# Optimization experiments

Hardware: AMD Instinct MI355X
Metric: run time of the kernel (lower is better)

Reference implementation:

```python
import jax, jax.numpy as jnp
import numpy as np

HIDDEN = 2048
N_HEADS = 16
HEAD_DIM = HIDDEN // N_HEADS
SEQ = 4096
ROPE_BASE = 10000.0


def setup_inputs() -> dict:
    key = jax.random.key(0)
    ks = jax.random.split(key, 5)
    sc = 1.0 / np.sqrt(HIDDEN)
    return {
        "hidden_states": jax.random.normal(ks[0], (SEQ, HIDDEN), jnp.float32),
        "Wq": jax.random.normal(ks[1], (HIDDEN, HIDDEN), jnp.float32) * sc,
        "Wk": jax.random.normal(ks[2], (HIDDEN, HIDDEN), jnp.float32) * sc,
        "Wv": jax.random.normal(ks[3], (HIDDEN, HIDDEN), jnp.float32) * sc,
        "Wo": jax.random.normal(ks[4], (HIDDEN, HIDDEN), jnp.float32) * sc,
    }


def _rope_cos_sin(seq_len, head_dim, dtype):
    # Llama-style rotary embedding tables, shape [S, 1, head_dim]
    inv_freq = 1.0 / (ROPE_BASE ** (jnp.arange(0, head_dim, 2, dtype=jnp.float32) / head_dim))
    pos = jnp.arange(seq_len, dtype=jnp.float32)
    freqs = pos[:, None] * inv_freq[None, :]          # [S, d/2]
    emb = jnp.concatenate([freqs, freqs], axis=-1)     # [S, d]
    return jnp.cos(emb)[:, None, :].astype(dtype), jnp.sin(emb)[:, None, :].astype(dtype)


def _rotate_half(x):
    h = x.shape[-1] // 2
    return jnp.concatenate([-x[..., h:], x[..., :h]], axis=-1)


def reference(hidden_states, Wq, Wk, Wv, Wo):
    S, H = hidden_states.shape
    d = HEAD_DIM
    # QKV projections (nn.Linear: x @ W.T), split into heads: [S, nH, d]
    q = (hidden_states @ Wq.T).reshape(S, N_HEADS, d)
    k = (hidden_states @ Wk.T).reshape(S, N_HEADS, d)
    v = (hidden_states @ Wv.T).reshape(S, N_HEADS, d)
    # Per-position RoPE on q and k
    cos, sin = _rope_cos_sin(S, d, q.dtype)
    q = q * cos + _rotate_half(q) * sin
    k = k * cos + _rotate_half(k) * sin
    # Causal scaled-dot-product attention, scores [nH, S, S]
    scores = jnp.einsum("snd,tnd->nst", q, k) / jnp.sqrt(jnp.asarray(d, q.dtype))
    causal = jnp.tril(jnp.ones((S, S), dtype=bool))
    scores = jnp.where(causal[None, :, :], scores, jnp.asarray(-1e30, scores.dtype))
    probs = jax.nn.softmax(scores, axis=-1)
    ctx = jnp.einsum("nst,tnd->snd", probs, v).reshape(S, H)
    return ctx @ Wo.T
```

## Files before the change

### kernel.cpp

```cpp
#include <hip/hip_runtime.h>

#define SEQ 4096
#define HIDDEN 2048
#define NHEADS 16
#define HDIM 128
#define QBLK 128
#define KVB 64

typedef float f32x4 __attribute__((ext_vector_type(4)));
typedef __bf16 bf16x8 __attribute__((ext_vector_type(8)));
typedef unsigned int u32x4 __attribute__((ext_vector_type(4)));
typedef unsigned short u16x8 __attribute__((ext_vector_type(8)));
typedef unsigned short u16;

#define SCL2 0.12751747456918851f
#define RLOG 0.2076205059304601f

__device__ __forceinline__ u16 f2bf(float f) {
  unsigned u = __float_as_uint(f);
  unsigned r = 0x7fffu + ((u >> 16) & 1u);
  return (u16)((u + r) >> 16);
}
__device__ __forceinline__ float bf2f(u16 u) {
  return __uint_as_float(((unsigned)u) << 16);
}
__device__ __forceinline__ unsigned cvtpk(float a, float b) {
  unsigned r;
  asm volatile("v_cvt_pk_bf16_f32 %0, %1, %2" : "=v"(r) : "v"(a), "v"(b));
  return r;
}

__device__ __forceinline__ void gload16(const u16* g, u16* l) {
  __builtin_amdgcn_global_load_lds(
      (const __attribute__((address_space(1))) unsigned int*)g,
      (__attribute__((address_space(3))) unsigned int*)l, 16, 0, 0);
}

__device__ __forceinline__ int cumq(int q) {
  return q < 24 ? (q - 12) * 2 : 24 + (q - 24) * 3;
}

__global__ __launch_bounds__(256) void cvt5(const float* __restrict__ X,
    const float* __restrict__ Wq, const float* __restrict__ Wk,
    const float* __restrict__ Wv, const float* __restrict__ Wo,
    u16* __restrict__ dst) {
  const size_t SH = (size_t)SEQ * HIDDEN, HH = (size_t)HIDDEN * HIDDEN;
  size_t i = ((size_t)blockIdx.x * 256 + threadIdx.x) * 8;
  const float* src; size_t off;
  if (i < SH) { src = X; off = i; }
  else if (i < SH + HH) { src = Wq; off = i - SH; }
  else if (i < SH + 2 * HH) { src = Wk; off = i - SH - HH; }
  else if (i < SH + 3 * HH) { src = Wv; off = i - SH - 2 * HH; }
  else { src = Wo; off = i - SH - 3 * HH; }
  float4 a = *reinterpret_cast<const float4*>(src + off);
  float4 b = *reinterpret_cast<const float4*>(src + off + 4);
  u16x8 o;
  o[0] = f2bf(a.x); o[1] = f2bf(a.y); o[2] = f2bf(a.z); o[3] = f2bf(a.w);
  o[4] = f2bf(b.x); o[5] = f2bf(b.y); o[6] = f2bf(b.z); o[7] = f2bf(b.w);
  *reinterpret_cast<u32x4*>(dst + i) = __builtin_bit_cast(u32x4, o);
}

__global__ __launch_bounds__(256, 3) void gemm_qkv(const u16* __restrict__ Xb,
    const u16* __restrict__ Wqb, const u16* __restrict__ Wkb,
    const u16* __restrict__ Wvb, u16* __restrict__ Qo, u16* __restrict__ Ko,
    u16* __restrict__ Vt) {
  __shared__ u16 As[3][4096];
  __shared__ u16 Bs[3][4096];
  const int wg = blockIdx.x;
  const int swz = (wg & 7) * 192 + (wg >> 3);
  const int z = swz >> 9;
  const int rr_ = swz & 511;
  const u16 *A, *B;
  u16* C;
  int bm, bn, cst;
  if (z == 2) {
    A = Wvb; B = Xb; C = Vt;
    bm = (rr_ & 15) << 7; bn = (rr_ >> 4) << 7; cst = SEQ;
  } else {
    A = Xb; B = z ? Wkb : Wqb; C = z ? Ko : Qo;
    bm = (rr_ & 31) << 7; bn = (rr_ >> 5) << 7; cst = HIDDEN;
  }
  const int t = threadIdx.x, lane = t & 63, wave = t >> 6;
  const int lrow = lane & 15, lgrp = lane >> 4;
  const int wr = (wave >> 1) * 64;
  const int wc = (wave & 1) * 64;
  const int r0 = t >> 2;
  const int c0 = ((t & 3) ^ ((r0 >> 1) & 3)) * 8;
  const int ksx8 = (lgrp ^ ((lrow >> 1) & 3)) * 8;

  f32x4 acc[4][4] = {};

  const u16* Ab = A + (size_t)(bm + r0) * HIDDEN + c0;
  const int nr0 = (z < 2)
      ? (((r0 >> 4) >> 1) * 16 + (r0 & 15) + ((r0 >> 4) & 1) * 64)
      : r0;
  const u16* Bb = B + (size_t)(bn + nr0) * HIDDEN + c0;
  const size_t rstepA = (size_t)64 * HIDDEN;
  const size_t rstepB = (size_t)((z < 2) ? 32 : 64) * HIDDEN;

#define QKV_STAGE(tt, s)                                            \
  {                                                                 \
    const int ko = (tt) * 32;                                       \
    gload16(Ab + ko, &As[s][t * 8]);                                \
    gload16(Bb + ko, &Bs[s][t * 8]);                                \
    gload16(Ab + rstepA + ko, &As[s][2048 + t * 8]);                \
    gload16(Bb + rstepB + ko, &Bs[s][2048 + t * 8]);                \
  }

  QKV_STAGE(0, 0);
  QKV_STAGE(1, 1);
  asm volatile("s_waitcnt vmcnt(4)" ::: "memory");
  __builtin_amdgcn_s_barrier();
  asm volatile("" ::: "memory");

  int sa = 0, sb = 1, sc = 2;
  for (int tt = 0; tt < 64; ++tt) {
    if (tt + 2 < 64) QKV_STAGE(tt + 2, sc);
    bf16x8 af[4], bfv[4];
#pragma unroll
    for (int mf = 0; mf < 4; ++mf)
      af[mf] = __builtin_bit_cast(bf16x8,
          *reinterpret_cast<const u32x4*>(&As[sa][(wr + mf * 16 + lrow) * 32 + ksx8]));
#pragma unroll
    for (int nf = 0; nf < 4; ++nf)
      bfv[nf] = __builtin_bit_cast(bf16x8,
          *reinterpret_cast<const u32x4*>(&Bs[sa][(wc + nf * 16 + lrow) * 32 + ksx8]));
#pragma unroll
    for (int nf = 0; nf < 4; ++nf)
#pragma unroll
      for (int mf = 0; mf < 4; ++mf)
        acc[mf][nf] = __builtin_amdgcn_mfma_f32_16x16x32_bf16(af[mf], bfv[nf], acc[mf][nf], 0, 0, 0);
    asm volatile("s_waitcnt vmcnt(4)" ::: "memory");
    __builtin_amdgcn_sched_barrier(0);
    __builtin_amdgcn_s_barrier();
    asm volatile("" ::: "memory");
    int s_ = sa; sa = sb; sb = sc; sc = s_;
  }
#undef QKV_STAGE

  const int rb = lgrp * 4;
  if (z < 2) {
    const float qscale = (z == 0) ? SCL2 : 1.0f;
#pragma unroll
    for (int mf = 0; mf < 4; ++mf)
#pragma unroll
      for (int j = 0; j < 2; ++j) {
        const int ii = (((wc >> 4) + 2 * j) >> 1) * 16 + lrow;
        const float inv = exp2f((float)ii * -RLOG);
#pragma unroll
        for (int qq = 0; qq < 4; ++qq) {
          const int s = bm + wr + mf * 16 + rb + qq;
          float ang = (float)s * inv;
          float sn, cs;
          __sincosf(ang, &sn, &cs);
          sn *= qscale; cs *= qscale;
          float x1 = acc[mf][2 * j][qq], x2 = acc[mf][2 * j + 1][qq];
          C[(size_t)s * cst + bn + ii] = f2bf(x1 * cs - x2 * sn);
          C[(size_t)s * cst + bn + ii + 64] = f2bf(x2 * cs + x1 * sn);
        }
      }
  } else {
#pragma unroll
    for (int mf = 0; mf < 4; ++mf)
#pragma unroll
      for (int nf = 0; nf < 4; ++nf) {
        const int col = bn + wc + ((nf >> 1) & 1) * 32 + (lrow >> 2) * 8 +
                        (nf & 1) * 4 + (lrow & 3);
#pragma unroll
        for (int qq = 0; qq < 4; ++qq) {
          const int s = bm + wr + mf * 16 + rb + qq;
          C[(size_t)s * cst + col] = f2bf(acc[mf][nf][qq]);
        }
      }
  }
}

__global__ __launch_bounds__(256, 3) void gemm_out(const u16* __restrict__ A,
    const u16* __restrict__ B, float* __restrict__ C) {
  __shared__ u16 As[3][4096];
  __shared__ u16 Bs[3][4096];
  const int wg = blockIdx.x;
  const int swz = (wg & 7) * 64 + (wg >> 3);
  const int bm = (swz & 31) << 7;
  const int bn = (swz >> 5) << 7;
  const int t = threadIdx.x, lane = t & 63, wave = t >> 6;
  const int lrow = lane & 15, lgrp = lane >> 4;
  const int wr = (wave >> 1) * 64;
  const int wc = (wave & 1) * 64;
  const int r0 = t >> 2;
  const int c0 = ((t & 3) ^ ((r0 >> 1) & 3)) * 8;
  const int ksx8 = (lgrp ^ ((lrow >> 1) & 3)) * 8;

  f32x4 acc[4][4] = {};

  const u16* Ab = A + (size_t)(bm + r0) * HIDDEN + c0;
  const u16* Bb = B + (size_t)(bn + r0) * HIDDEN + c0;
  const size_t rstep = (size_t)64 * HIDDEN;

#define OUT_STAGE(tt, s)                                            \
  {                                                                 \
    const int ko = (tt) * 32;                                       \
    gload16(Ab + ko, &As[s][t * 8]);                                \
    gload16(Bb + ko, &Bs[s][t * 8]);                                \
    gload16(Ab + rstep + ko, &As[s][2048 + t * 8]);                 \
    gload16(Bb + rstep + ko, &Bs[s][2048 + t * 8]);                 \
  }

  OUT_STAGE(0, 0);
  OUT_STAGE(1, 1);
  asm volatile("s_waitcnt vmcnt(4)" ::: "memory");
  __builtin_amdgcn_s_barrier();
  asm volatile("" ::: "memory");

  int sa = 0, sb = 1, sc = 2;
  for (int tt = 0; tt < 64; ++tt) {
    if (tt + 2 < 64) OUT_STAGE(tt + 2, sc);
    bf16x8 af[4], bfv[4];
#pragma unroll
    for (int mf = 0; mf < 4; ++mf)
      af[mf] = __builtin_bit_cast(bf16x8,
          *reinterpret_cast<const u32x4*>(&As[sa][(wr + mf * 16 + lrow) * 32 + ksx8]));
#pragma unroll
    for (int nf = 0; nf < 4; ++nf)
      bfv[nf] = __builtin_bit_cast(bf16x8,
          *reinterpret_cast<const u32x4*>(&Bs[sa][(wc + nf * 16 + lrow) * 32 + ksx8]));
#pragma unroll
    for (int nf = 0; nf < 4; ++nf)
#pragma unroll
      for (int mf = 0; mf < 4; ++mf)
        acc[mf][nf] = __builtin_amdgcn_mfma_f32_16x16x32_bf16(af[mf], bfv[nf], acc[mf][nf], 0, 0, 0);
    asm volatile("s_waitcnt vmcnt(4)" ::: "memory");
    __builtin_amdgcn_sched_barrier(0);
    __builtin_amdgcn_s_barrier();
    asm volatile("" ::: "memory");
    int s_ = sa; sa = sb; sb = sc; sc = s_;
  }
#undef OUT_STAGE

  const int rb = lgrp * 4;
#pragma unroll
  for (int mf = 0; mf < 4; ++mf)
#pragma unroll
    for (int nf = 0; nf < 4; ++nf)
#pragma unroll
      for (int qq = 0; qq < 4; ++qq)
        C[(size_t)(bm + wr + mf * 16 + rb + qq) * HIDDEN + bn + wc + nf * 16 + lrow] =
            acc[mf][nf][qq];
}

__global__ __launch_bounds__(512, 4) void attn_kernel(const u16* __restrict__ Q,
                                                      const u16* __restrict__ Kg,
                                                      const u16* __restrict__ Vt,
                                                      u16* __restrict__ O,
                                                      u16* __restrict__ Opart,
                                                      float* __restrict__ Ml) {
  __shared__ u16 Ks[2][KVB * 128];
  __shared__ u16 Vs[2][128 * KVB];
  const int t = threadIdx.x;
  const int wave = t >> 6;
  const int lane = t & 63;
  const int lrow = lane & 15;
  const int lgrp = lane >> 4;

  const int g = blockIdx.x;
  const int h = g & 15;
  const int e = g >> 4;
  int q, c, nc;
  if (e < 24)      { q = 24 + e / 3;           c = e % 3;         nc = 3; }
  else if (e < 48) { q = 23 - ((e - 24) >> 1); c = (e - 24) & 1;  nc = 2; }
  else             { q = 59 - e;               c = 0;             nc = 1; }
  const int total = 2 * q + 2;
  const int base = total / nc, rem = total - base * nc;
  const int it0 = c * base + (c < rem ? c : rem);
  const int it1 = it0 + base + (c < rem ? 1 : 0);

  const int qw = q * QBLK + wave * 16;

  bf16x8 qf[4];
#pragma unroll
  for (int kk = 0; kk < 4; ++kk)
    qf[kk] = __builtin_bit_cast(bf16x8, *reinterpret_cast<const u32x4*>(
        Q + (size_t)(qw + lrow) * HIDDEN + h * HDIM + kk * 32 + lgrp * 8));

  u16x8 ow;
#pragma unroll
  for (int j = 0; j < 8; ++j) ow[j] = (lrow == 0) ? 0x3F80 : 0;
  const bf16x8 vones = __builtin_bit_cast(bf16x8, ow);

  const u16* kgb[2]; const u16* vgb[2]; int kof[2], vof[2];
#pragma unroll
  for (int is = 0; is < 2; ++is) {
    int ch = is * 512 + t;
    int krow = ch >> 4, kslot = ch & 15;
    int kcol = ((kslot & 8) | ((kslot ^ krow) & 7)) * 8;
    kgb[is] = Kg + (size_t)krow * HIDDEN + h * HDIM + kcol;
    kof[is] = ch * 8;
    int vrow = ch >> 3, vslot = ch & 7;
    int vcol = ((vslot ^ vrow) & 7) * 8;
    vgb[is] = Vt + (size_t)(h * HDIM + vrow) * SEQ + vcol;
    vof[is] = ch * 8;
  }

  f32x4 acc[8] = {};
  f32x4 acc1 = {};
  float m2 = -1e30f;

#pragma unroll
  for (int is = 0; is < 2; ++is) {
    gload16(kgb[is] + (size_t)(it0 * KVB) * HIDDEN, &Ks[0][kof[is]]);
    gload16(vgb[is] + it0 * KVB, &Vs[0][vof[is]]);
  }
  __syncthreads();

  int p = 0;
  for (int bt = it0; bt < it1; ++bt) {
    const int t0 = bt * KVB;
    if (bt + 1 < it1) {
      const int t1 = (bt + 1) * KVB;
#pragma unroll
      for (int is = 0; is < 2; ++is) {
        gload16(kgb[is] + (size_t)t1 * HIDDEN, &Ks[p ^ 1][kof[is]]);
        gload16(vgb[is] + t1, &Vs[p ^ 1][vof[is]]);
      }
    }

    if (t0 <= qw + 15) {
      const bool need_mask = (t0 + KVB - 1 > qw);
      f32x4 sc[4] = {};
      __builtin_amdgcn_s_setprio(1);
#pragma unroll
      for (int kk = 0; kk < 4; ++kk) {
#pragma unroll
        for (int colf = 0; colf < 4; ++colf) {
          int trow = colf * 16 + lrow;
          int slot = kk * 4 + lgrp;
          bf16x8 kf = __builtin_bit_cast(bf16x8, *reinterpret_cast<const u32x4*>(
              &Ks[p][trow * 128 + ((slot & 8) | ((slot ^ trow) & 7)) * 8]));
          sc[colf] = __builtin_amdgcn_mfma_f32_16x16x32_bf16(kf, qf[kk], sc[colf], 0, 0, 0);
        }
      }
      __builtin_amdgcn_s_setprio(0);

      const int qg = qw + lrow;
      if (need_mask) {
#pragma unroll
        for (int colf = 0; colf < 4; ++colf) {
          const int kvb0 = t0 + colf * 16 + lgrp * 4;
#pragma unroll
          for (int r = 0; r < 4; ++r)
            sc[colf][r] = (kvb0 + r <= qg) ? sc[colf][r] : -1e30f;
        }
      }
      float mc[4];
#pragma unroll
      for (int colf = 0; colf < 4; ++colf)
        mc[colf] = fmaxf(fmaxf(sc[colf][0], sc[colf][1]),
                         fmaxf(sc[colf][2], sc[colf][3]));
      float mx = fmaxf(fmaxf(mc[0], mc[1]), fmaxf(mc[2], mc[3]));
      mx = fmaxf(mx, __shfl_xor(mx, 16));
      mx = fmaxf(mx, __shfl_xor(mx, 32));

      if (__any(mx > m2 + 11.5f)) {
        float mn = fmaxf(m2, mx);
        float sf = exp2f(m2 - mn);
        m2 = mn;
#pragma unroll
        for (int r = 0; r < 4; ++r) {
          float sfr = __shfl(sf, (lane & 48) | (lgrp * 4 + r));
#pragma unroll
          for (int nn = 0; nn < 8; ++nn) acc[nn][r] *= sfr;
          acc1[r] *= sfr;
        }
      }

      unsigned paw[2][4];
#pragma unroll
      for (int colf = 0; colf < 4; ++colf) {
        float pv[4];
#pragma unroll
        for (int r = 0; r < 4; ++r) pv[r] = exp2f(sc[colf][r] - m2);
        paw[colf >> 1][(colf & 1) * 2 + 0] = cvtpk(pv[0], pv[1]);
        paw[colf >> 1][(colf & 1) * 2 + 1] = cvtpk(pv[2], pv[3]);
      }

      __builtin_amdgcn_s_setprio(1);
#pragma unroll
      for (int ks = 0; ks < 2; ++ks) {
        u32x4 w = {paw[ks][0], paw[ks][1], paw[ks][2], paw[ks][3]};
        bf16x8 pa = __builtin_bit_cast(bf16x8, w);
#pragma unroll
        for (int nn = 0; nn < 8; ++nn) {
          const int d = nn * 16 + lrow;
          bf16x8 vb = __builtin_bit_cast(bf16x8, *reinterpret_cast<const u32x4*>(
              &Vs[p][d * 64 + (((ks * 4 + lgrp) ^ d) & 7) * 8]));
          acc[nn] = __builtin_amdgcn_mfma_f32_16x16x32_bf16(pa, vb, acc[nn], 0, 0, 0);
        }
        acc1 = __builtin_amdgcn_mfma_f32_16x16x32_bf16(pa, vones, acc1, 0, 0, 0);
      }
      __builtin_amdgcn_s_setprio(0);
    }

    __syncthreads();
    p ^= 1;
  }

  if (nc == 1) {
    float inv[4];
#pragma unroll
    for (int r = 0; r < 4; ++r)
      inv[r] = 1.0f / __shfl(acc1[r], lane & 48);
#pragma unroll
    for (int nn = 0; nn < 8; ++nn)
#pragma unroll
      for (int r = 0; r < 4; ++r) {
        int row = qw + lgrp * 4 + r;
        int col = h * HDIM + nn * 16 + lrow;
        O[(size_t)row * HIDDEN + col] = f2bf(acc[nn][r] * inv[r]);
      }
  } else {
    const int slot = h * 48 + cumq(q) + c;
    u16* Op = Opart + (size_t)slot * (QBLK * HDIM);
    float* ml = Ml + (size_t)slot * 256;
#pragma unroll
    for (int nn = 0; nn < 8; ++nn)
#pragma unroll
      for (int r = 0; r < 4; ++r) {
        int rl = wave * 16 + lgrp * 4 + r;
        Op[rl * HDIM + nn * 16 + lrow] = f2bf(acc[nn][r]);
      }
    if (lgrp == 0) {
      int rl = wave * 16 + lrow;
      ml[rl] = m2;
    }
    if (lrow == 0) {
#pragma unroll
      for (int r = 0; r < 4; ++r)
        ml[128 + wave * 16 + lgrp * 4 + r] = acc1[r];
    }
  }
}

__global__ __launch_bounds__(256) void combine_kernel(const u16* __restrict__ Opart,
                                                      const float* __restrict__ Ml,
                                                      u16* __restrict__ O) {
  const int bid = blockIdx.x;
  const int h = bid / 20;
  const int q = 12 + bid % 20;
  const int nc = (q < 24) ? 2 : 3;
  const int sbase = h * 48 + cumq(q);
  const int r = threadIdx.x >> 1;
  const int d0 = (threadIdx.x & 1) * 64;

  float w[3], l = 0.f, M = -3.0e38f;
#pragma unroll
  for (int c = 0; c < 3; ++c)
    if (c < nc) M = fmaxf(M, Ml[(size_t)(sbase + c) * 256 + r]);
#pragma unroll
  for (int c = 0; c < 3; ++c)
    if (c < nc) {
      w[c] = exp2f(Ml[(size_t)(sbase + c) * 256 + r] - M);
      l += w[c] * Ml[(size_t)(sbase + c) * 256 + 128 + r];
    }
  const float inv = 1.0f / l;

  for (int dd = 0; dd < 64; dd += 8) {
    float a8[8] = {};
#pragma unroll
    for (int c = 0; c < 3; ++c)
      if (c < nc) {
        u16x8 v = *reinterpret_cast<const u16x8*>(
            Opart + (size_t)(sbase + c) * (QBLK * HDIM) + r * HDIM + d0 + dd);
#pragma unroll
        for (int j = 0; j < 8; ++j) a8[j] += w[c] * bf2f(v[j]);
      }
    u16x8 o8;
#pragma unroll
    for (int j = 0; j < 8; ++j) o8[j] = f2bf(a8[j] * inv);
    *reinterpret_cast<u16x8*>(
        &O[(size_t)(q * QBLK + r) * HIDDEN + h * HDIM + d0 + dd]) = o8;
  }
}

extern "C" void kernel_launch(void* const* d_in, const int* in_sizes, int n_in,
                              void* d_out, int out_size, void* d_ws, size_t ws_size,
                              hipStream_t stream) {
  const float* X  = (const float*)d_in[0];
  const float* Wq = (const float*)d_in[1];
  const float* Wk = (const float*)d_in[2];
  const float* Wv = (const float*)d_in[3];
  const float* Wo = (const float*)d_in[4];
  float* out = (float*)d_out;

  u16* ws = (u16*)d_ws;
  const size_t SH = (size_t)SEQ * HIDDEN;
  const size_t HH = (size_t)HIDDEN * HIDDEN;
  u16* Xb  = ws;
  u16* Wqb = Xb + SH;
  u16* Wkb = Wqb + HH;
  u16* Wvb = Wkb + HH;
  u16* Wob = Wvb + HH;
  u16* Qb  = Wob + HH;
  u16* Kb  = Qb + SH;
  u16* Vtb = Kb + SH;
  u16* Cb  = Vtb + SH;

  u16* Opart = ws;
  float* Ml = (float*)(ws + (size_t)768 * 16384);

  cvt5<<<(int)((SH + 4 * HH) / 2048), 256, 0, stream>>>(X, Wq, Wk, Wv, Wo, ws);

  gemm_qkv<<<1536, 256, 0, stream>>>(Xb, Wqb, Wkb, Wvb, Qb, Kb, Vtb);

  attn_kernel<<<960, 512, 0, stream>>>(Qb, Kb, Vtb, Cb, Opart, Ml);
  combine_kernel<<<320, 256, 0, stream>>>(Opart, Ml, Cb);

  gemm_out<<<512, 256, 0, stream>>>(Cb, Wob, out);
}
```

Before: 323.1 us.

## Double attention query tile to 256 rows with two row fragments per wave

Each wave of the attention kernel now handles 32 query rows (two 16-row fragments) instead of 16, so every K/V tile loaded into shared memory feeds twice as many MFMAs. The split-KV schedule is rebuilt for 16 query tiles per head with up to 4 chunks, and the combine kernel and workspace layout are resized to match. This halves K/V traffic per query but doubles accumulator registers per wave, which may reduce occupancy under the 512x4 launch bounds, and it leaves fewer blocks (640 instead of 960).

Result: slower. 514.8 us (+59.3%).

```diff
diff --git a/kernel.cpp b/kernel.cpp
--- a/kernel.cpp
+++ b/kernel.cpp
@@ -4,7 +4,6 @@
 #define HIDDEN 2048
 #define NHEADS 16
 #define HDIM 128
-#define QBLK 128
 #define KVB 64
 
 typedef float f32x4 __attribute__((ext_vector_type(4)));
@@ -37,7 +36,9 @@
 }
 
 __device__ __forceinline__ int cumq(int q) {
-  return q < 24 ? (q - 12) * 2 : 24 + (q - 24) * 3;
+  if (q < 8) return (q - 4) * 2;
+  if (q < 12) return 8 + (q - 8) * 3;
+  return 20 + (q - 12) * 4;
 }
 
 __global__ __launch_bounds__(256) void cvt5(const float* __restrict__ X,
@@ -265,51 +266,46 @@
   const int g = blockIdx.x;
   const int h = g & 15;
   const int e = g >> 4;
-  int q, c, nc;
-  if (e < 24)      { q = 24 + e / 3;           c = e % 3;         nc = 3; }
-  else if (e < 48) { q = 23 - ((e - 24) >> 1); c = (e - 24) & 1;  nc = 2; }
-  else             { q = 59 - e;               c = 0;             nc = 1; }
-  const int total = 2 * q + 2;
+  int qt, c, nc;
+  if (e < 16)      { qt = 15 - (e >> 2);        c = e & 3;         nc = 4; }
+  else if (e < 28) { qt = 11 - (e - 16) / 3;    c = (e - 16) % 3;  nc = 3; }
+  else if (e < 36) { qt = 7 - ((e - 28) >> 1);  c = (e - 28) & 1;  nc = 2; }
+  else             { qt = 39 - e;               c = 0;             nc = 1; }
+  const int total = 4 * (qt + 1);
   const int base = total / nc, rem = total - base * nc;
   const int it0 = c * base + (c < rem ? c : rem);
   const int it1 = it0 + base + (c < rem ? 1 : 0);
 
-  const int qw = q * QBLK + wave * 16;
-
-  bf16x8 qf[4];
-#pragma unroll
-  for (int kk = 0; kk < 4; ++kk)
-    qf[kk] = __builtin_bit_cast(bf16x8, *reinterpret_cast<const u32x4*>(
-        Q + (size_t)(qw + lrow) * HIDDEN + h * HDIM + kk * 32 + lgrp * 8));
+  const int qw = qt * 256 + wave * 32;
+
+  bf16x8 qf[2][4];
+#pragma unroll
+  for (int rowf = 0; rowf < 2; ++rowf)
+#pragma unroll
+    for (int kk = 0; kk < 4; ++kk)
+      qf[rowf][kk] = __builtin_bit_cast(bf16x8, *reinterpret_cast<const u32x4*>(
+          Q + (size_t)(qw + rowf * 16 + lrow) * HIDDEN + h * HDIM + kk * 32 + lgrp * 8));
 
   u16x8 ow;
 #pragma unroll
   for (int j = 0; j < 8; ++j) ow[j] = (lrow == 0) ? 0x3F80 : 0;
   const bf16x8 vones = __builtin_bit_cast(bf16x8, ow);
 
-  const u16* kgb[2]; const u16* vgb[2]; int kof[2], vof[2];
-#pragma unroll
-  for (int is = 0; is < 2; ++is) {
-    int ch = is * 512 + t;
-    int krow = ch >> 4, kslot = ch & 15;
-    int kcol = ((kslot & 8) | ((kslot ^ krow) & 7)) * 8;
-    kgb[is] = Kg + (size_t)krow * HIDDEN + h * HDIM + kcol;
-    kof[is] = ch * 8;
-    int vrow = ch >> 3, vslot = ch & 7;
-    int vcol = ((vslot ^ vrow) & 7) * 8;
-    vgb[is] = Vt + (size_t)(h * HDIM + vrow) * SEQ + vcol;
-    vof[is] = ch * 8;
-  }
-
-  f32x4 acc[8] = {};
-  f32x4 acc1 = {};
-  float m2 = -1e30f;
-
-#pragma unroll
-  for (int is = 0; is < 2; ++is) {
-    gload16(kgb[is] + (size_t)(it0 * KVB) * HIDDEN, &Ks[0][kof[is]]);
-    gload16(vgb[is] + it0 * KVB, &Vs[0][vof[is]]);
-  }
+  const int krow = t >> 4, kslot = t & 15;
+  const int kcol = ((kslot & 8) | ((kslot ^ krow) & 7)) * 8;
+  const u16* kg0 = Kg + (size_t)krow * HIDDEN + h * HDIM + kcol;
+  const int vrow = t >> 3, vslot = t & 7;
+  const int vcol = ((vslot ^ vrow) & 7) * 8;
+  const u16* vg0 = Vt + (size_t)(h * HDIM + vrow) * SEQ + vcol;
+
+  f32x4 acc[2][8] = {};
+  f32x4 acc1[2] = {};
+  float m2[2] = {-1e30f, -1e30f};
+
+  gload16(kg0 + (size_t)(it0 * KVB) * HIDDEN, &Ks[0][t * 8]);
+  gload16(kg0 + (size_t)(it0 * KVB + 32) * HIDDEN, &Ks[0][4096 + t * 8]);
+  gload16(vg0 + it0 * KVB, &Vs[0][t * 8]);
+  gload16(vg0 + (size_t)64 * SEQ + it0 * KVB, &Vs[0][4096 + t * 8]);
   __syncthreads();
 
   int p = 0;
@@ -317,16 +313,15 @@
     const int t0 = bt * KVB;
     if (bt + 1 < it1) {
       const int t1 = (bt + 1) * KVB;
-#pragma unroll
-      for (int is = 0; is < 2; ++is) {
-        gload16(kgb[is] + (size_t)t1 * HIDDEN, &Ks[p ^ 1][kof[is]]);
-        gload16(vgb[is] + t1, &Vs[p ^ 1][vof[is]]);
-      }
+      gload16(kg0 + (size_t)t1 * HIDDEN, &Ks[p ^ 1][t * 8]);
+      gload16(kg0 + (size_t)(t1 + 32) * HIDDEN, &Ks[p ^ 1][4096 + t * 8]);
+      gload16(vg0 + t1, &Vs[p ^ 1][t * 8]);
+      gload16(vg0 + (size_t)64 * SEQ + t1, &Vs[p ^ 1][4096 + t * 8]);
     }
 
-    if (t0 <= qw + 15) {
+    if (t0 <= qw + 31) {
       const bool need_mask = (t0 + KVB - 1 > qw);
-      f32x4 sc[4] = {};
+      f32x4 sc[2][4] = {};
       __builtin_amdgcn_s_setprio(1);
 #pragma unroll
       for (int kk = 0; kk < 4; ++kk) {
@@ -336,66 +331,91 @@
           int slot = kk * 4 + lgrp;
           bf16x8 kf = __builtin_bit_cast(bf16x8, *reinterpret_cast<const u32x4*>(
               &Ks[p][trow * 128 + ((slot & 8) | ((slot ^ trow) & 7)) * 8]));
-          sc[colf] = __builtin_amdgcn_mfma_f32_16x16x32_bf16(kf, qf[kk], sc[colf], 0, 0, 0);
+#pragma unroll
+          for (int rowf = 0; rowf < 2; ++rowf)
+            sc[rowf][colf] = __builtin_amdgcn_mfma_f32_16x16x32_bf16(
+                kf, qf[rowf][kk], sc[rowf][colf], 0, 0, 0);
         }
       }
       __builtin_amdgcn_s_setprio(0);
 
-      const int qg = qw + lrow;
-      if (need_mask) {
+      float pmax[2];
+#pragma unroll
+      for (int rowf = 0; rowf < 2; ++rowf) {
+        const int qg = qw + rowf * 16 + lrow;
+        if (need_mask) {
+#pragma unroll
+          for (int colf = 0; colf < 4; ++colf) {
+            const int kvb0 = t0 + colf * 16 + lgrp * 4;
+#pragma unroll
+            for (int r = 0; r < 4; ++r)
+              sc[rowf][colf][r] = (kvb0 + r <= qg) ? sc[rowf][colf][r] : -1e30f;
+          }
+        }
+        float mc[4];
+#pragma unroll
+        for (int colf = 0; colf < 4; ++colf)
+          mc[colf] = fmaxf(fmaxf(sc[rowf][colf][0], sc[rowf][colf][1]),
+                           fmaxf(sc[rowf][colf][2], sc[rowf][colf][3]));
+        float mx = fmaxf(fmaxf(mc[0], mc[1]), fmaxf(mc[2], mc[3]));
+        mx = fmaxf(mx, __shfl_xor(mx, 16));
+        mx = fmaxf(mx, __shfl_xor(mx, 32));
+        pmax[rowf] = mx;
+      }
+
+      bool grow = (pmax[0] > m2[0] + 11.5f) || (pmax[1] > m2[1] + 11.5f);
+      if (__any(grow)) {
+#pragma unroll
+        for (int rowf = 0; rowf < 2; ++rowf) {
+          float mn = fmaxf(m2[rowf], pmax[rowf]);
+          float sf = exp2f(m2[rowf] - mn);
+          m2[rowf] = mn;
+#pragma unroll
+          for (int r = 0; r < 4; ++r) {
+            float sfr = __shfl(sf, (lane & 48) | (lgrp * 4 + r));
+#pragma unroll
+            for (int nn = 0; nn < 8; ++nn) acc[rowf][nn][r] *= sfr;
+            acc1[rowf][r] *= sfr;
+          }
+        }
+      }
+
+      unsigned paw[2][2][4];
+#pragma unroll
+      for (int rowf = 0; rowf < 2; ++rowf)
 #pragma unroll
         for (int colf = 0; colf < 4; ++colf) {
-          const int kvb0 = t0 + colf * 16 + lgrp * 4;
-#pragma unroll
-          for (int r = 0; r < 4; ++r)
-            sc[colf][r] = (kvb0 + r <= qg) ? sc[colf][r] : -1e30f;
-        }
-      }
-      float mc[4];
-#pragma unroll
-      for (int colf = 0; colf < 4; ++colf)
-        mc[colf] = fmaxf(fmaxf(sc[colf][0], sc[colf][1]),
-                         fmaxf(sc[colf][2], sc[colf][3]));
-      float mx = fmaxf(fmaxf(mc[0], mc[1]), fmaxf(mc[2], mc[3]));
-      mx = fmaxf(mx, __shfl_xor(mx, 16));
-      mx = fmaxf(mx, __shfl_xor(mx, 32));
-
-      if (__any(mx > m2 + 11.5f)) {
-        float mn = fmaxf(m2, mx);
-        float sf = exp2f(m2 - mn);
-        m2 = mn;
-#pragma unroll
-        for (int r = 0; r < 4; ++r) {
-          float sfr = __shfl(sf, (lane & 48) | (lgrp * 4 + r));
-#pragma unroll
-          for (int nn = 0; nn < 8; ++nn) acc[nn][r] *= sfr;
-          acc1[r] *= sfr;
-        }
-      }
-
-      unsigned paw[2][4];
-#pragma unroll
-      for (int colf = 0; colf < 4; ++colf) {
-        float pv[4];
-#pragma unroll
-        for (int r = 0; r < 4; ++r) pv[r] = exp2f(sc[colf][r] - m2);
-        paw[colf >> 1][(colf & 1) * 2 + 0] = cvtpk(pv[0], pv[1]);
-        paw[colf >> 1][(colf & 1) * 2 + 1] = cvtpk(pv[2], pv[3]);
-      }
+          float pv[4];
+#pragma unroll
+          for (int r = 0; r < 4; ++r) pv[r] = exp2f(sc[rowf][colf][r] - m2[rowf]);
+          paw[rowf][colf >> 1][(colf & 1) * 2 + 0] = cvtpk(pv[0], pv[1]);
+          paw[rowf][colf >> 1][(colf & 1) * 2 + 1] = cvtpk(pv[2], pv[3]);
+        }
 
       __builtin_amdgcn_s_setprio(1);
 #pragma unroll
       for (int ks = 0; ks < 2; ++ks) {
-        u32x4 w = {paw[ks][0], paw[ks][1], paw[ks][2], paw[ks][3]};
-        bf16x8 pa = __builtin_bit_cast(bf16x8, w);
+        bf16x8 pa[2];
+#pragma unroll
+        for (int rowf = 0; rowf < 2; ++rowf) {
+          u32x4 w = {paw[rowf][ks][0], paw[rowf][ks][1],
+                     paw[rowf][ks][2], paw[rowf][ks][3]};
+          pa[rowf] = __builtin_bit_cast(bf16x8, w);
+        }
 #pragma unroll
         for (int nn = 0; nn < 8; ++nn) {
           const int d = nn * 16 + lrow;
           bf16x8 vb = __builtin_bit_cast(bf16x8, *reinterpret_cast<const u32x4*>(
               &Vs[p][d * 64 + (((ks * 4 + lgrp) ^ d) & 7) * 8]));
-          acc[nn] = __builtin_amdgcn_mfma_f32_16x16x32_bf16(pa, vb, acc[nn], 0, 0, 0);
-        }
-        acc1 = __builtin_amdgcn_mfma_f32_16x16x32_bf16(pa, vones, acc1, 0, 0, 0);
+#pragma unroll
+          for (int rowf = 0; rowf < 2; ++rowf)
+            acc[rowf][nn] = __builtin_amdgcn_mfma_f32_16x16x32_bf16(
+                pa[rowf], vb, acc[rowf][nn], 0, 0, 0);
+        }
+#pragma unroll
+        for (int rowf = 0; rowf < 2; ++rowf)
+          acc1[rowf] = __builtin_amdgcn_mfma_f32_16x16x32_bf16(
+              pa[rowf], vones, acc1[rowf], 0, 0, 0);
       }
       __builtin_amdgcn_s_setprio(0);
     }
@@ -405,37 +425,41 @@
   }
 
   if (nc == 1) {
-    float inv[4];
-#pragma unroll
-    for (int r = 0; r < 4; ++r)
-      inv[r] = 1.0f / __shfl(acc1[r], lane & 48);
-#pragma unroll
-    for (int nn = 0; nn < 8; ++nn)
-#pragma unroll
-      for (int r = 0; r < 4; ++r) {
-        int row = qw + lgrp * 4 + r;
-        int col = h * HDIM + nn * 16 + lrow;
-        O[(size_t)row * HIDDEN + col] = f2bf(acc[nn][r] * inv[r]);
-      }
+#pragma unroll
+    for (int rowf = 0; rowf < 2; ++rowf) {
+      float inv[4];
+#pragma unroll
+      for (int r = 0; r < 4; ++r)
+        inv[r] = 1.0f / __shfl(acc1[rowf][r], lane & 48);
+#pragma unroll
+      for (int nn = 0; nn < 8; ++nn)
+#pragma unroll
+        for (int r = 0; r < 4; ++r) {
+          int row = qw + rowf * 16 + lgrp * 4 + r;
+          int col = h * HDIM + nn * 16 + lrow;
+          O[(size_t)row * HIDDEN + col] = f2bf(acc[rowf][nn][r] * inv[r]);
+        }
+    }
   } else {
-    const int slot = h * 48 + cumq(q) + c;
-    u16* Op = Opart + (size_t)slot * (QBLK * HDIM);
-    float* ml = Ml + (size_t)slot * 256;
-#pragma unroll
-    for (int nn = 0; nn < 8; ++nn)
-#pragma unroll
-      for (int r = 0; r < 4; ++r) {
-        int rl = wave * 16 + lgrp * 4 + r;
-        Op[rl * HDIM + nn * 16 + lrow] = f2bf(acc[nn][r]);
-      }
-    if (lgrp == 0) {
-      int rl = wave * 16 + lrow;
-      ml[rl] = m2;
-    }
-    if (lrow == 0) {
-#pragma unroll
-      for (int r = 0; r < 4; ++r)
-        ml[128 + wave * 16 + lgrp * 4 + r] = acc1[r];
+    const int slot = h * 36 + cumq(qt) + c;
+    u16* Op = Opart + (size_t)slot * (256 * HDIM);
+    float* ml = Ml + (size_t)slot * 512;
+#pragma unroll
+    for (int rowf = 0; rowf < 2; ++rowf) {
+#pragma unroll
+      for (int nn = 0; nn < 8; ++nn)
+#pragma unroll
+        for (int r = 0; r < 4; ++r) {
+          int rl = wave * 32 + rowf * 16 + lgrp * 4 + r;
+          Op[rl * HDIM + nn * 16 + lrow] = f2bf(acc[rowf][nn][r]);
+        }
+      if (lgrp == 0)
+        ml[wave * 32 + rowf * 16 + lrow] = m2[rowf];
+      if (lrow == 0) {
+#pragma unroll
+        for (int r = 0; r < 4; ++r)
+          ml[256 + wave * 32 + rowf * 16 + lgrp * 4 + r] = acc1[rowf][r];
+      }
     }
   }
 }
@@ -444,32 +468,31 @@
                                                       const float* __restrict__ Ml,
                                                       u16* __restrict__ O) {
   const int bid = blockIdx.x;
-  const int h = bid / 20;
-  const int q = 12 + bid % 20;
-  const int nc = (q < 24) ? 2 : 3;
-  const int sbase = h * 48 + cumq(q);
-  const int r = threadIdx.x >> 1;
-  const int d0 = (threadIdx.x & 1) * 64;
-
-  float w[3], l = 0.f, M = -3.0e38f;
-#pragma unroll
-  for (int c = 0; c < 3; ++c)
-    if (c < nc) M = fmaxf(M, Ml[(size_t)(sbase + c) * 256 + r]);
-#pragma unroll
-  for (int c = 0; c < 3; ++c)
+  const int h = bid / 12;
+  const int q = 4 + bid % 12;
+  const int nc = (q < 8) ? 2 : ((q < 12) ? 3 : 4);
+  const int sbase = h * 36 + cumq(q);
+  const int r = threadIdx.x;
+
+  float w[4], l = 0.f, M = -3.0e38f;
+#pragma unroll
+  for (int c = 0; c < 4; ++c)
+    if (c < nc) M = fmaxf(M, Ml[(size_t)(sbase + c) * 512 + r]);
+#pragma unroll
+  for (int c = 0; c < 4; ++c)
     if (c < nc) {
-      w[c] = exp2f(Ml[(size_t)(sbase + c) * 256 + r] - M);
-      l += w[c] * Ml[(size_t)(sbase + c) * 256 + 128 + r];
+      w[c] = exp2f(Ml[(size_t)(sbase + c) * 512 + r] - M);
+      l += w[c] * Ml[(size_t)(sbase + c) * 512 + 256 + r];
     }
   const float inv = 1.0f / l;
 
-  for (int dd = 0; dd < 64; dd += 8) {
+  for (int dd = 0; dd < 128; dd += 8) {
     float a8[8] = {};
 #pragma unroll
-    for (int c = 0; c < 3; ++c)
+    for (int c = 0; c < 4; ++c)
       if (c < nc) {
         u16x8 v = *reinterpret_cast<const u16x8*>(
-            Opart + (size_t)(sbase + c) * (QBLK * HDIM) + r * HDIM + d0 + dd);
+            Opart + (size_t)(sbase + c) * (256 * HDIM) + r * HDIM + dd);
 #pragma unroll
         for (int j = 0; j < 8; ++j) a8[j] += w[c] * bf2f(v[j]);
       }
@@ -477,7 +500,7 @@
 #pragma unroll
     for (int j = 0; j < 8; ++j) o8[j] = f2bf(a8[j] * inv);
     *reinterpret_cast<u16x8*>(
-        &O[(size_t)(q * QBLK + r) * HIDDEN + h * HDIM + d0 + dd]) = o8;
+        &O[(size_t)(q * 256 + r) * HIDDEN + h * HDIM + dd]) = o8;
   }
 }
 
@@ -505,14 +528,14 @@
   u16* Cb  = Vtb + SH;
 
   u16* Opart = ws;
-  float* Ml = (float*)(ws + (size_t)768 * 16384);
+  float* Ml = (float*)(ws + (size_t)576 * 32768);
 
   cvt5<<<(int)((SH + 4 * HH) / 2048), 256, 0, stream>>>(X, Wq, Wk, Wv, Wo, ws);
 
   gemm_qkv<<<1536, 256, 0, stream>>>(Xb, Wqb, Wkb, Wvb, Qb, Kb, Vtb);
 
-  attn_kernel<<<960, 512, 0, stream>>>(Qb, Kb, Vtb, Cb, Opart, Ml);
-  combine_kernel<<<320, 256, 0, stream>>>(Opart, Ml, Cb);
+  attn_kernel<<<640, 512, 0, stream>>>(Qb, Kb, Vtb, Cb, Opart, Ml);
+  combine_kernel<<<192, 256, 0, stream>>>(Opart, Ml, Cb);
 
   gemm_out<<<512, 256, 0, stream>>>(Cb, Wob, out);
 }
```
